# Optimization experiments

Measured on AMD Instinct MI355X. Metric: run time of the kernel, lower is better.

The kernel has to match this reference:

```python
import jax, jax.numpy as jnp
import numpy as np

EMBED = 256
PC_RANGE = np.array([-51.2, -51.2, -5.0, 51.2, 51.2, 3.0], np.float32)
INF_PC_RANGE = np.array([0.0, -51.2, -5.0, 102.4, 51.2, 3.0], np.float32)
EPS = 1e-5
NUM_THINGS = 3
THRESHOLD = 0.05


def _inverse_sigmoid(x):
    # mmdet inverse_sigmoid with eps=1e-5
    x = jnp.clip(x, 0.0, 1.0)
    x1 = jnp.clip(x, EPS, None)
    x2 = jnp.clip(1.0 - x, EPS, None)
    return jnp.log(x1 / x2)


def _norm2lidar(locs, pc_range):
    lo = jnp.asarray(pc_range[:3])
    hi = jnp.asarray(pc_range[3:])
    return locs * (hi - lo) + lo


def _lidar2norm(locs, pc_range):
    lo = jnp.asarray(pc_range[:3])
    hi = jnp.asarray(pc_range[3:])
    return (locs - lo) / (hi - lo)


def _transform(pts, calib):
    # pts [..., 3]; homogeneous transform with calib [4,4]
    h = jnp.concatenate([pts, jnp.ones_like(pts[..., :1])], -1)
    return jnp.einsum('ij,...j->...i', calib, h)[..., :3]


def setup_inputs() -> dict:
    key = jax.random.key(0)
    ks = jax.random.split(key, 16)
    L, BS, NI, NV, C = 6, 1, 8192, 16384, 3
    # logits shifted positive so sigmoid > 0.05 for every (query, class):
    # matching torch's duplicate-index gather semantics).
    inf_cls = jnp.abs(jax.random.normal(ks[0], (L, BS, NI, C), jnp.float32)) + 0.2
    inp = {
        'inf_outputs_classes': inf_cls,
        'inf_outputs_coords': jax.random.uniform(ks[1], (L, BS, NI, 4), jnp.float32),
        'inf_query': jax.random.normal(ks[2], (BS, NI, EMBED), jnp.float32),
        'inf_query_pos': jax.random.normal(ks[3], (BS, NI, EMBED), jnp.float32),
        'inf_reference': jax.random.normal(ks[4], (BS, NI, 4), jnp.float32),
        'veh_outputs_classes': jax.random.normal(ks[5], (L, BS, NV, C), jnp.float32),
        'veh_outputs_coords': jax.random.uniform(ks[6], (L, BS, NV, 4), jnp.float32),
        'veh_query': jax.random.normal(ks[7], (BS, NV, EMBED), jnp.float32),
        'veh_query_pos': jax.random.normal(ks[8], (BS, NV, EMBED), jnp.float32),
        'veh_reference': jax.random.normal(ks[9], (BS, NV, 4), jnp.float32),
    }
    # valid rigid inf->veh calibration T; module computes calib = inv(veh2inf_rt[0].T)
    th = 0.3
    T = np.eye(4, dtype=np.float64)
    T[:3, :3] = [[np.cos(th), -np.sin(th), 0.0], [np.sin(th), np.cos(th), 0.0], [0.0, 0.0, 1.0]]
    T[:3, 3] = [10.0, 2.0, 0.5]
    inp['veh2inf_rt'] = jnp.asarray(np.linalg.inv(T).T, jnp.float32)[None]
    s = 0.05
    inp['W_align'] = jax.random.normal(ks[10], (EMBED + 9, EMBED), jnp.float32) * s
    inp['b_align'] = jax.random.normal(ks[11], (EMBED,), jnp.float32) * s
    inp['W_align_pos'] = jax.random.normal(ks[12], (EMBED + 9, EMBED), jnp.float32) * s
    inp['b_align_pos'] = jax.random.normal(ks[13], (EMBED,), jnp.float32) * s
    return inp


def reference(inf_outputs_classes, inf_outputs_coords, inf_query, inf_query_pos,
              inf_reference, veh_outputs_classes, veh_outputs_coords, veh_query,
              veh_query_pos, veh_reference, veh2inf_rt, W_align, b_align,
              W_align_pos, b_align_pos):
    # calibration goes through numpy in the original -> constant, non-differentiable
    calib = jnp.asarray(np.linalg.inv(np.asarray(veh2inf_rt[0], np.float64).T), jnp.float32)

    # ---- filter_inf_lanes: threshold on last-layer sigmoid scores ----
    cls_score = jax.nn.sigmoid(inf_outputs_classes[-1])            # [bs, N, C]
    indexes = jnp.nonzero(cls_score.reshape(-1) > THRESHOLD)[0]
    bbox_index = indexes // NUM_THINGS                              # duplicates kept

    inf_outputs_classes = inf_outputs_classes[:, :, bbox_index, :]
    inf_outputs_coords = inf_outputs_coords[:, :, bbox_index, :]
    inf_query = inf_query[:, bbox_index, :]
    inf_query_pos = inf_query_pos[:, bbox_index, :]
    inf_reference = inf_reference[:, bbox_index, :]

    # ---- reference points: inf norm -> inf lidar -> veh lidar -> veh norm ----
    ref3 = jnp.concatenate([inf_reference[..., :2],
                            jnp.zeros_like(inf_reference[..., :1])], -1)  # [bs,N,3]
    locs = jax.nn.sigmoid(ref3)                    # _norm2lidar inverse_sigmoid mode
    locs = _norm2lidar(locs, INF_PC_RANGE)
    locs = _transform(locs, calib)
    locs = _inverse_sigmoid(_lidar2norm(locs, PC_RANGE))
    inf_reference = inf_reference.at[..., :2].set(locs[..., :2])

    # ---- per-layer bbox centers: same transform in sigmoid space ----
    bb3 = jnp.concatenate([inf_outputs_coords[..., :2],
                           jnp.zeros_like(inf_outputs_coords[..., :1])], -1)  # [L,bs,N,3]
    bb3 = _norm2lidar(bb3, INF_PC_RANGE)
    bb3 = _transform(bb3, calib)
    bb3 = _lidar2norm(bb3, PC_RANGE)
    inf_outputs_coords = inf_outputs_coords.at[..., :2].set(bb3[..., :2])

    # ---- cross-agent query alignment with rotation conditioning ----
    r = calib[:3, :3].reshape(9)
    r_b = jnp.broadcast_to(r, inf_query.shape[:-1] + (9,))
    inf_query = jnp.concatenate([inf_query, r_b], -1) @ W_align + b_align
    inf_query_pos = jnp.concatenate([inf_query_pos, r_b], -1) @ W_align_pos + b_align_pos

    # ---- complement vehicle-side sets with aligned inf lanes ----
    outputs_classes = jnp.concatenate([veh_outputs_classes, inf_outputs_classes], axis=2)
    outputs_coords = jnp.concatenate([veh_outputs_coords, inf_outputs_coords], axis=2)
    query = jnp.concatenate([veh_query, inf_query], axis=1)
    query_pos = jnp.concatenate([veh_query_pos, inf_query_pos], axis=1)
    reference = jnp.concatenate([veh_reference, inf_reference], axis=1)
    return (outputs_classes, outputs_coords, query, query_pos, reference)
```

## Files before the change

### kernel.cpp

```cpp
#include <hip/hip_runtime.h>
#include <hip/hip_bf16.h>

#define EMBED 256
#define LL 6

typedef __attribute__((ext_vector_type(8))) __bf16 bf16x8;
typedef __attribute__((ext_vector_type(4))) float f32x4;

#define SEL_THR (-2.9444389791664403f)

__global__ __launch_bounds__(1024) void k12(
        const float* __restrict__ cls, int n,
        const float* __restrict__ rt,
        const float* __restrict__ W0, const float* __restrict__ W1,
        const float* __restrict__ b0, const float* __restrict__ b1,
        float* __restrict__ calib,
        int* __restrict__ bbox, int* __restrict__ cnt,
        __bf16* __restrict__ Wt0, __bf16* __restrict__ Wt1,
        float* __restrict__ bvec0, float* __restrict__ bvec1) {
    int tid = threadIdx.x;

    if (blockIdx.x != 0) {
        int idx0 = blockIdx.x - 1;
        int which = idx0 >> 4;
        int t = idx0 & 15;
        int k0 = (t >> 2) * 64, c0 = (t & 3) * 64;
        const float* W = which ? W1 : W0;
        __bf16* Wt     = which ? Wt1 : Wt0;
        __shared__ float T[64][65];
#pragma unroll
        for (int i = 0; i < 4; ++i) {
            int idx = i * 1024 + tid;
            int kk = idx >> 6, cc = idx & 63;
            T[kk][cc] = W[(size_t)(k0 + kk) * EMBED + c0 + cc];
        }
        __syncthreads();
#pragma unroll
        for (int i = 0; i < 4; ++i) {
            int idx = i * 1024 + tid;
            int cc = idx >> 6, kk = idx & 63;
            Wt[(size_t)(c0 + cc) * EMBED + k0 + kk] = (__bf16)T[kk][cc];
        }
        return;
    }

    __shared__ int warpCnt[16];
    __shared__ float s_calib[16];
    int wid = tid >> 6, lane = tid & 63;

    if (tid == 0) {
        double a[4][8];
        for (int i = 0; i < 4; ++i)
            for (int j = 0; j < 4; ++j) {
                a[i][j]     = (double)rt[j * 4 + i];
                a[i][4 + j] = (i == j) ? 1.0 : 0.0;
            }
        for (int c = 0; c < 4; ++c) {
            int p = c; double best = fabs(a[c][c]);
            for (int r = c + 1; r < 4; ++r) { double v = fabs(a[r][c]); if (v > best) { best = v; p = r; } }
            if (p != c) for (int j = 0; j < 8; ++j) { double t2 = a[c][j]; a[c][j] = a[p][j]; a[p][j] = t2; }
            double inv = 1.0 / a[c][c];
            for (int j = 0; j < 8; ++j) a[c][j] *= inv;
            for (int r = 0; r < 4; ++r) if (r != c) {
                double f = a[r][c];
                for (int j = 0; j < 8; ++j) a[r][j] -= f * a[c][j];
            }
        }
        for (int i = 0; i < 4; ++i)
            for (int j = 0; j < 4; ++j) {
                float v = (float)a[i][4 + j];
                calib[i * 4 + j] = v;
                s_calib[i * 4 + j] = v;
            }
    }

    int PT = ((n + 1023) / 1024 + 3) & ~3;
    int PT4 = PT >> 2;
    int start = tid * PT;

    float4 v[16];
#pragma unroll
    for (int j4 = 0; j4 < 16; ++j4) {
        if (j4 < PT4) {
            int s = start + j4 * 4;
            if (s + 4 <= n) {
                v[j4] = *(const float4*)&cls[s];
            } else {
                float4 t2; t2.x = t2.y = t2.z = t2.w = -1e30f;
                if (s + 0 < n) t2.x = cls[s + 0];
                if (s + 1 < n) t2.y = cls[s + 1];
                if (s + 2 < n) t2.z = cls[s + 2];
                if (s + 3 < n) t2.w = cls[s + 3];
                v[j4] = t2;
            }
        }
    }
    int c = 0;
#pragma unroll
    for (int j4 = 0; j4 < 16; ++j4) {
        if (j4 < PT4) {
            c += (v[j4].x > SEL_THR) + (v[j4].y > SEL_THR) +
                 (v[j4].z > SEL_THR) + (v[j4].w > SEL_THR);
        }
    }
    int incl = c;
#pragma unroll
    for (int off = 1; off < 64; off <<= 1) {
        int u = __shfl_up(incl, off, 64);
        if (lane >= off) incl += u;
    }
    if (lane == 63) warpCnt[wid] = incl;
    __syncthreads();

    int base = 0;
    for (int w2 = 0; w2 < wid; ++w2) base += warpCnt[w2];
    int pos = base + incl - c;
#pragma unroll
    for (int j4 = 0; j4 < 16; ++j4) {
        if (j4 < PT4) {
            int s = start + j4 * 4;
            if (s + 0 < n && v[j4].x > SEL_THR) bbox[pos++] = (s + 0) / 3;
            if (s + 1 < n && v[j4].y > SEL_THR) bbox[pos++] = (s + 1) / 3;
            if (s + 2 < n && v[j4].z > SEL_THR) bbox[pos++] = (s + 2) / 3;
            if (s + 3 < n && v[j4].w > SEL_THR) bbox[pos++] = (s + 3) / 3;
        }
    }
    if (tid == 0) {
        int tot = 0;
        for (int w2 = 0; w2 < 16; ++w2) tot += warpCnt[w2];
        *cnt = tot;
    }

    if (tid < 512) {
        int which = tid >> 8;
        int j = tid & 255;
        const float* W = which ? W1 : W0;
        const float* b = which ? b1 : b0;
        float* o       = which ? bvec1 : bvec0;
        float s = b[j];
#pragma unroll
        for (int u = 0; u < 9; ++u) {
            float r = s_calib[(u / 3) * 4 + (u % 3)];
            s += r * W[(EMBED + u) * EMBED + j];
        }
        o[j] = s;
    }
}

__device__ __forceinline__ bf16x8 cvt8(float4 f0, float4 f1) {
    bf16x8 r;
    r[0] = (__bf16)f0.x; r[1] = (__bf16)f0.y; r[2] = (__bf16)f0.z; r[3] = (__bf16)f0.w;
    r[4] = (__bf16)f1.x; r[5] = (__bf16)f1.y; r[6] = (__bf16)f1.z; r[7] = (__bf16)f1.w;
    return r;
}

__global__ __launch_bounds__(256, 4) void k_gemm(
        const float* __restrict__ q0, const float* __restrict__ q1,
        const int* __restrict__ bbox,
        const __bf16* __restrict__ Wt0, const __bf16* __restrict__ Wt1,
        const float* __restrict__ bvec0, const float* __restrict__ bvec1,
        float* __restrict__ out, int NI, int K, int off0, int off1) {
    int g = blockIdx.y;
    const float* q    = g ? q1 : q0;
    const __bf16* Wt  = g ? Wt1 : Wt0;
    const float* bvec = g ? bvec1 : bvec0;
    int out_off       = g ? off1 : off0;

    int tid  = threadIdx.x;
    int w    = tid >> 6;
    int lane = tid & 63;
    int lo16 = lane & 15;
    int kg   = lane >> 4;
    int r0 = blockIdx.x * 64;

    const float* aptr[4];
#pragma unroll
    for (int t = 0; t < 4; ++t) {
        int row = r0 + 16 * t + lo16;
        int rc = min(row, K - 1);
        int box = bbox[rc]; box = max(0, min(box, NI - 1));
        aptr[t] = q + (size_t)box * EMBED + kg * 8;
    }
    const __bf16* bptr[4];
#pragma unroll
    for (int t = 0; t < 4; ++t) {
        int col = w * 64 + 16 * t + lo16;
        bptr[t] = Wt + (size_t)col * EMBED + kg * 8;
    }

    f32x4 acc[4][4];
#pragma unroll
    for (int ct = 0; ct < 4; ++ct) {
        float bv = bvec[w * 64 + 16 * ct + lo16];
#pragma unroll
        for (int rt = 0; rt < 4; ++rt) {
            acc[rt][ct][0] = bv; acc[rt][ct][1] = bv; acc[rt][ct][2] = bv; acc[rt][ct][3] = bv;
        }
    }
    for (int s = 0; s < 8; ++s) {
        bf16x8 a[4], b[4];
#pragma unroll
        for (int t = 0; t < 4; ++t) {
            float4 f0 = *(const float4*)(aptr[t] + s * 32);
            float4 f1 = *(const float4*)(aptr[t] + s * 32 + 4);
            a[t] = cvt8(f0, f1);
            b[t] = *(const bf16x8*)(bptr[t] + s * 32);
        }
#pragma unroll
        for (int rt = 0; rt < 4; ++rt)
#pragma unroll
            for (int ct = 0; ct < 4; ++ct)
                acc[rt][ct] = __builtin_amdgcn_mfma_f32_16x16x32_bf16(a[rt], b[ct], acc[rt][ct], 0, 0, 0);
    }
#pragma unroll
    for (int rt = 0; rt < 4; ++rt) {
#pragma unroll
        for (int reg = 0; reg < 4; ++reg) {
            int row = r0 + 16 * rt + kg * 4 + reg;
            if (row < K) {
#pragma unroll
                for (int ct = 0; ct < 4; ++ct) {
                    int col = w * 64 + 16 * ct + lo16;
                    out[out_off + (size_t)row * EMBED + col] = acc[rt][ct][reg];
                }
            }
        }
    }
}

struct Plan3 {
    const float* vsrc[5];
    const float* isrc[3];
    int start[9];
    int n4[5];
    int vdst[5];
    int idst[3];
    int perLay4[2];
    int layStride[2];
    int K, NI, NV, N;
};

__device__ __forceinline__ float inv_sig(float v) {
    v = fminf(fmaxf(v, 0.0f), 1.0f);
    float x1 = fmaxf(v, 1e-5f);
    float x2 = fmaxf(1.0f - v, 1e-5f);
    return logf(x1 / x2);
}

__global__ __launch_bounds__(256) void k3(Plan3 P, const int* __restrict__ bbox,
                                          const float* __restrict__ calib,
                                          float* __restrict__ out) {
    int bx = blockIdx.x;
    int j = 0;
    while (bx >= P.start[j + 1]) ++j;
    int lb  = bx - P.start[j];
    int tid = threadIdx.x;

    if (j < 5) {
        const int cmap[5] = {2, 3, 0, 1, 4};
        int cj = cmap[j];
#pragma unroll
        for (int it = 0; it < 4; ++it) {
            int i4 = lb * 1024 + it * 256 + tid;
            if (i4 < P.n4[cj]) {
                float4 v = *(const float4*)&P.vsrc[cj][(size_t)i4 * 4];
                size_t d;
                if (cj < 2) {
                    int l = i4 / P.perLay4[cj];
                    int r = i4 - l * P.perLay4[cj];
                    d = (size_t)P.vdst[cj] + (size_t)l * P.layStride[cj] + (size_t)r * 4;
                } else {
                    d = (size_t)P.vdst[cj] + (size_t)i4 * 4;
                }
                *(float4*)&out[d] = v;
            }
        }
        return;
    }

    int k = lb * 256 + tid;
    if (k >= P.K) return;
    int box = bbox[k]; box = max(0, min(box, P.NI - 1));

    if (j == 5) {
        const float* s0 = P.isrc[0];
#pragma unroll
        for (int l = 0; l < LL; ++l) {
            const float* s = s0 + ((size_t)l * P.NI + box) * 3;
            size_t d = (size_t)P.idst[0] + ((size_t)l * P.N + P.NV) * 3 + (size_t)k * 3;
            out[d + 0] = s[0]; out[d + 1] = s[1]; out[d + 2] = s[2];
        }
    } else if (j == 6) {
        float c00 = calib[0], c01 = calib[1], c03 = calib[3];
        float c10 = calib[4], c11 = calib[5], c13 = calib[7];
        float zx = calib[2] * -5.0f, zy = calib[6] * -5.0f;
#pragma unroll
        for (int l = 0; l < LL; ++l) {
            float4 s = *(const float4*)&P.isrc[1][((size_t)l * P.NI + box) * 4];
            float X = s.x * 102.4f;
            float Y = s.y * 102.4f - 51.2f;
            float tx = c00 * X + c01 * Y + zx + c03;
            float ty = c10 * X + c11 * Y + zy + c13;
            float4 v = make_float4((tx + 51.2f) * (1.0f / 102.4f),
                                   (ty + 51.2f) * (1.0f / 102.4f), s.z, s.w);
            *(float4*)&out[(size_t)P.idst[1] + ((size_t)l * P.N + P.NV + k) * 4] = v;
        }
    } else {
        float4 s = *(const float4*)&P.isrc[2][(size_t)box * 4];
        float sx = 1.0f / (1.0f + expf(-s.x));
        float sy = 1.0f / (1.0f + expf(-s.y));
        float X = sx * 102.4f;
        float Y = sy * 102.4f - 51.2f;
        float tx = calib[0] * X + calib[1] * Y + calib[2] * -1.0f + calib[3];
        float ty = calib[4] * X + calib[5] * Y + calib[6] * -1.0f + calib[7];
        float4 v = make_float4(inv_sig((tx + 51.2f) * (1.0f / 102.4f)),
                               inv_sig((ty + 51.2f) * (1.0f / 102.4f)), s.z, s.w);
        *(float4*)&out[(size_t)P.idst[2] + ((size_t)P.NV + k) * 4] = v;
    }
}

extern "C" void kernel_launch(void* const* d_in, const int* in_sizes, int n_in,
                              void* d_out, int out_size, void* d_ws, size_t ws_size,
                              hipStream_t stream) {
    const float* inf_cls   = (const float*)d_in[0];
    const float* inf_coord = (const float*)d_in[1];
    const float* inf_q     = (const float*)d_in[2];
    const float* inf_qp    = (const float*)d_in[3];
    const float* inf_ref   = (const float*)d_in[4];
    const float* veh_cls   = (const float*)d_in[5];
    const float* veh_coord = (const float*)d_in[6];
    const float* veh_q     = (const float*)d_in[7];
    const float* veh_qp    = (const float*)d_in[8];
    const float* veh_ref   = (const float*)d_in[9];
    const float* rt        = (const float*)d_in[10];
    const float* W0        = (const float*)d_in[11];
    const float* b0        = (const float*)d_in[12];
    const float* W1        = (const float*)d_in[13];
    const float* b1        = (const float*)d_in[14];
    float* out = (float*)d_out;

    int NI = in_sizes[0] / (LL * 3);
    int NV = in_sizes[5] / (LL * 3);
    int N  = out_size / 558;
    int K  = N - NV;

    int off_cls   = 0;
    int off_coord = LL * N * 3;
    int off_q     = off_coord + LL * N * 4;
    int off_qp    = off_q + N * EMBED;
    int off_ref   = off_qp + N * EMBED;

    char* ws = (char*)d_ws;
    float* calib = (float*)(ws);
    float* bvec0 = (float*)(ws + 128);
    float* bvec1 = (float*)(ws + 1152);
    int*   cnt   = (int*)(ws + 2176);
    int*   bbox  = (int*)(ws + 2304);
    __bf16* Wt0  = (__bf16*)(ws + 131072);
    __bf16* Wt1  = (__bf16*)(ws + 262144);

    hipLaunchKernelGGL(k12, dim3(33), dim3(1024), 0, stream,
                       inf_cls + (size_t)(LL - 1) * NI * 3, NI * 3, rt,
                       W0, W1, b0, b1, calib, bbox, cnt, Wt0, Wt1, bvec0, bvec1);

    if (K > 0) {
        hipLaunchKernelGGL(k_gemm, dim3((K + 63) / 64, 2), dim3(256), 0, stream,
                           inf_q, inf_qp, bbox, Wt0, Wt1, bvec0, bvec1,
                           out, NI, K, off_q + NV * EMBED, off_qp + NV * EMBED);
    }

    {
        Plan3 P;
        P.vsrc[0] = veh_cls; P.vsrc[1] = veh_coord; P.vsrc[2] = veh_q;
        P.vsrc[3] = veh_qp;  P.vsrc[4] = veh_ref;
        P.isrc[0] = inf_cls; P.isrc[1] = inf_coord; P.isrc[2] = inf_ref;
        P.n4[0] = LL * NV * 3 / 4;  P.n4[1] = LL * NV * 4 / 4;
        P.n4[2] = NV * EMBED / 4;   P.n4[3] = NV * EMBED / 4;  P.n4[4] = NV * 4 / 4;
        P.vdst[0] = off_cls; P.vdst[1] = off_coord; P.vdst[2] = off_q;
        P.vdst[3] = off_qp;  P.vdst[4] = off_ref;
        P.idst[0] = off_cls; P.idst[1] = off_coord; P.idst[2] = off_ref;
        P.perLay4[0] = NV * 3 / 4;  P.perLay4[1] = NV * 4 / 4;
        P.layStride[0] = N * 3;     P.layStride[1] = N * 4;
        P.K = K; P.NI = NI; P.NV = NV; P.N = N;

        int gblk = (K > 0) ? (K + 255) / 256 : 0;
        int nb[8];
        nb[0] = (P.n4[2] + 1023) / 1024;
        nb[1] = (P.n4[3] + 1023) / 1024;
        nb[2] = (P.n4[0] + 1023) / 1024;
        nb[3] = (P.n4[1] + 1023) / 1024;
        nb[4] = (P.n4[4] + 1023) / 1024;
        nb[5] = gblk; nb[6] = gblk; nb[7] = gblk;
        P.start[0] = 0;
        for (int j = 0; j < 8; ++j) P.start[j + 1] = P.start[j] + nb[j];
        if (P.start[8] > 0) {
            hipLaunchKernelGGL(k3, dim3(P.start[8]), dim3(256), 0, stream,
                               P, bbox, calib, out);
        }
    }
}
```

Measured before the change: 66.10 us.

## Shrink prep kernel to 256 threads and use grid-stride 2D copy kernel

```diff
diff --git a/kernel.cpp b/kernel.cpp
--- a/kernel.cpp
+++ b/kernel.cpp
@@ -8,8 +8,9 @@
 typedef __attribute__((ext_vector_type(4))) float f32x4;
 
 #define SEL_THR (-2.9444389791664403f)
-
-__global__ __launch_bounds__(1024) void k12(
+#define MAXPT4 32
+
+__global__ __launch_bounds__(256, 1) void k_prep(
         const float* __restrict__ cls, int n,
         const float* __restrict__ rt,
         const float* __restrict__ W0, const float* __restrict__ W1,
@@ -29,22 +30,22 @@
         __bf16* Wt     = which ? Wt1 : Wt0;
         __shared__ float T[64][65];
 #pragma unroll
-        for (int i = 0; i < 4; ++i) {
-            int idx = i * 1024 + tid;
+        for (int i = 0; i < 16; ++i) {
+            int idx = i * 256 + tid;
             int kk = idx >> 6, cc = idx & 63;
             T[kk][cc] = W[(size_t)(k0 + kk) * EMBED + c0 + cc];
         }
         __syncthreads();
 #pragma unroll
-        for (int i = 0; i < 4; ++i) {
-            int idx = i * 1024 + tid;
+        for (int i = 0; i < 16; ++i) {
+            int idx = i * 256 + tid;
             int cc = idx >> 6, kk = idx & 63;
             Wt[(size_t)(c0 + cc) * EMBED + k0 + kk] = (__bf16)T[kk][cc];
         }
         return;
     }
 
-    __shared__ int warpCnt[16];
+    __shared__ int warpCnt[4];
     __shared__ float s_calib[16];
     int wid = tid >> 6, lane = tid & 63;
 
@@ -74,13 +75,13 @@
             }
     }
 
-    int PT = ((n + 1023) / 1024 + 3) & ~3;
+    int PT = ((n + 255) / 256 + 3) & ~3;
     int PT4 = PT >> 2;
     int start = tid * PT;
 
-    float4 v[16];
-#pragma unroll
-    for (int j4 = 0; j4 < 16; ++j4) {
+    float4 v[MAXPT4];
+#pragma unroll
+    for (int j4 = 0; j4 < MAXPT4; ++j4) {
         if (j4 < PT4) {
             int s = start + j4 * 4;
             if (s + 4 <= n) {
@@ -97,7 +98,7 @@
     }
     int c = 0;
 #pragma unroll
-    for (int j4 = 0; j4 < 16; ++j4) {
+    for (int j4 = 0; j4 < MAXPT4; ++j4) {
         if (j4 < PT4) {
             c += (v[j4].x > SEL_THR) + (v[j4].y > SEL_THR) +
                  (v[j4].z > SEL_THR) + (v[j4].w > SEL_THR);
@@ -116,7 +117,7 @@
     for (int w2 = 0; w2 < wid; ++w2) base += warpCnt[w2];
     int pos = base + incl - c;
 #pragma unroll
-    for (int j4 = 0; j4 < 16; ++j4) {
+    for (int j4 = 0; j4 < MAXPT4; ++j4) {
         if (j4 < PT4) {
             int s = start + j4 * 4;
             if (s + 0 < n && v[j4].x > SEL_THR) bbox[pos++] = (s + 0) / 3;
@@ -127,23 +128,22 @@
     }
     if (tid == 0) {
         int tot = 0;
-        for (int w2 = 0; w2 < 16; ++w2) tot += warpCnt[w2];
+        for (int w2 = 0; w2 < 4; ++w2) tot += warpCnt[w2];
         *cnt = tot;
     }
 
-    if (tid < 512) {
-        int which = tid >> 8;
-        int j = tid & 255;
+#pragma unroll
+    for (int which = 0; which < 2; ++which) {
         const float* W = which ? W1 : W0;
         const float* b = which ? b1 : b0;
         float* o       = which ? bvec1 : bvec0;
-        float s = b[j];
+        float s = b[tid];
 #pragma unroll
         for (int u = 0; u < 9; ++u) {
             float r = s_calib[(u / 3) * 4 + (u % 3)];
-            s += r * W[(EMBED + u) * EMBED + j];
-        }
-        o[j] = s;
+            s += r * W[(EMBED + u) * EMBED + tid];
+        }
+        o[tid] = s;
     }
 }
 
@@ -228,15 +228,11 @@
     }
 }
 
-struct Plan3 {
-    const float* vsrc[5];
-    const float* isrc[3];
-    int start[9];
-    int n4[5];
-    int vdst[5];
-    int idst[3];
-    int perLay4[2];
-    int layStride[2];
+struct SJob { const float* src; int n4; int dstOff; int perLay4; int layStride; };
+struct PlanS {
+    SJob cj[5];
+    const float* icls; const float* icoord; const float* iref;
+    int dcls, dcoord, dref;
     int K, NI, NV, N;
 };
 
@@ -247,75 +243,68 @@
     return logf(x1 / x2);
 }
 
-__global__ __launch_bounds__(256) void k3(Plan3 P, const int* __restrict__ bbox,
-                                          const float* __restrict__ calib,
-                                          float* __restrict__ out) {
-    int bx = blockIdx.x;
-    int j = 0;
-    while (bx >= P.start[j + 1]) ++j;
-    int lb  = bx - P.start[j];
+__global__ __launch_bounds__(256) void k_stream(PlanS P, const int* __restrict__ bbox,
+                                                const float* __restrict__ calib,
+                                                float* __restrict__ out) {
+    int y = blockIdx.y;
     int tid = threadIdx.x;
 
-    if (j < 5) {
-        const int cmap[5] = {2, 3, 0, 1, 4};
-        int cj = cmap[j];
-#pragma unroll
-        for (int it = 0; it < 4; ++it) {
-            int i4 = lb * 1024 + it * 256 + tid;
-            if (i4 < P.n4[cj]) {
-                float4 v = *(const float4*)&P.vsrc[cj][(size_t)i4 * 4];
-                size_t d;
-                if (cj < 2) {
-                    int l = i4 / P.perLay4[cj];
-                    int r = i4 - l * P.perLay4[cj];
-                    d = (size_t)P.vdst[cj] + (size_t)l * P.layStride[cj] + (size_t)r * 4;
-                } else {
-                    d = (size_t)P.vdst[cj] + (size_t)i4 * 4;
-                }
-                *(float4*)&out[d] = v;
+    if (y < 5) {
+        SJob J = P.cj[y];
+        int stride = gridDim.x * 256;
+        if (J.layStride == 0) {
+            for (int i4 = blockIdx.x * 256 + tid; i4 < J.n4; i4 += stride) {
+                float4 v = *(const float4*)&J.src[(size_t)i4 * 4];
+                *(float4*)&out[(size_t)J.dstOff + (size_t)i4 * 4] = v;
+            }
+        } else {
+            for (int i4 = blockIdx.x * 256 + tid; i4 < J.n4; i4 += stride) {
+                int l = i4 / J.perLay4;
+                int r = i4 - l * J.perLay4;
+                float4 v = *(const float4*)&J.src[(size_t)i4 * 4];
+                *(float4*)&out[(size_t)J.dstOff + (size_t)l * J.layStride + (size_t)r * 4] = v;
             }
         }
         return;
     }
 
-    int k = lb * 256 + tid;
-    if (k >= P.K) return;
-    int box = bbox[k]; box = max(0, min(box, P.NI - 1));
-
-    if (j == 5) {
-        const float* s0 = P.isrc[0];
-#pragma unroll
-        for (int l = 0; l < LL; ++l) {
-            const float* s = s0 + ((size_t)l * P.NI + box) * 3;
-            size_t d = (size_t)P.idst[0] + ((size_t)l * P.N + P.NV) * 3 + (size_t)k * 3;
-            out[d + 0] = s[0]; out[d + 1] = s[1]; out[d + 2] = s[2];
-        }
-    } else if (j == 6) {
-        float c00 = calib[0], c01 = calib[1], c03 = calib[3];
-        float c10 = calib[4], c11 = calib[5], c13 = calib[7];
-        float zx = calib[2] * -5.0f, zy = calib[6] * -5.0f;
-#pragma unroll
-        for (int l = 0; l < LL; ++l) {
-            float4 s = *(const float4*)&P.isrc[1][((size_t)l * P.NI + box) * 4];
-            float X = s.x * 102.4f;
-            float Y = s.y * 102.4f - 51.2f;
-            float tx = c00 * X + c01 * Y + zx + c03;
-            float ty = c10 * X + c11 * Y + zy + c13;
-            float4 v = make_float4((tx + 51.2f) * (1.0f / 102.4f),
-                                   (ty + 51.2f) * (1.0f / 102.4f), s.z, s.w);
-            *(float4*)&out[(size_t)P.idst[1] + ((size_t)l * P.N + P.NV + k) * 4] = v;
-        }
-    } else {
-        float4 s = *(const float4*)&P.isrc[2][(size_t)box * 4];
-        float sx = 1.0f / (1.0f + expf(-s.x));
-        float sy = 1.0f / (1.0f + expf(-s.y));
-        float X = sx * 102.4f;
-        float Y = sy * 102.4f - 51.2f;
-        float tx = calib[0] * X + calib[1] * Y + calib[2] * -1.0f + calib[3];
-        float ty = calib[4] * X + calib[5] * Y + calib[6] * -1.0f + calib[7];
-        float4 v = make_float4(inv_sig((tx + 51.2f) * (1.0f / 102.4f)),
-                               inv_sig((ty + 51.2f) * (1.0f / 102.4f)), s.z, s.w);
-        *(float4*)&out[(size_t)P.idst[2] + ((size_t)P.NV + k) * 4] = v;
+    int stride = gridDim.x * 256;
+    for (int k = blockIdx.x * 256 + tid; k < P.K; k += stride) {
+        int box = bbox[k]; box = max(0, min(box, P.NI - 1));
+        if (y == 5) {
+#pragma unroll
+            for (int l = 0; l < LL; ++l) {
+                const float* s = P.icls + ((size_t)l * P.NI + box) * 3;
+                size_t d = (size_t)P.dcls + ((size_t)l * P.N + P.NV) * 3 + (size_t)k * 3;
+                out[d + 0] = s[0]; out[d + 1] = s[1]; out[d + 2] = s[2];
+            }
+        } else if (y == 6) {
+            float c00 = calib[0], c01 = calib[1], c03 = calib[3];
+            float c10 = calib[4], c11 = calib[5], c13 = calib[7];
+            float zx = calib[2] * -5.0f, zy = calib[6] * -5.0f;
+#pragma unroll
+            for (int l = 0; l < LL; ++l) {
+                float4 s = *(const float4*)&P.icoord[((size_t)l * P.NI + box) * 4];
+                float X = s.x * 102.4f;
+                float Y = s.y * 102.4f - 51.2f;
+                float tx = c00 * X + c01 * Y + zx + c03;
+                float ty = c10 * X + c11 * Y + zy + c13;
+                float4 v = make_float4((tx + 51.2f) * (1.0f / 102.4f),
+                                       (ty + 51.2f) * (1.0f / 102.4f), s.z, s.w);
+                *(float4*)&out[(size_t)P.dcoord + ((size_t)l * P.N + P.NV + k) * 4] = v;
+            }
+        } else {
+            float4 s = *(const float4*)&P.iref[(size_t)box * 4];
+            float sx = 1.0f / (1.0f + expf(-s.x));
+            float sy = 1.0f / (1.0f + expf(-s.y));
+            float X = sx * 102.4f;
+            float Y = sy * 102.4f - 51.2f;
+            float tx = calib[0] * X + calib[1] * Y + calib[2] * -1.0f + calib[3];
+            float ty = calib[4] * X + calib[5] * Y + calib[6] * -1.0f + calib[7];
+            float4 v = make_float4(inv_sig((tx + 51.2f) * (1.0f / 102.4f)),
+                                   inv_sig((ty + 51.2f) * (1.0f / 102.4f)), s.z, s.w);
+            *(float4*)&out[(size_t)P.dref + ((size_t)P.NV + k) * 4] = v;
+        }
     }
 }
 
@@ -359,7 +348,7 @@
     __bf16* Wt0  = (__bf16*)(ws + 131072);
     __bf16* Wt1  = (__bf16*)(ws + 262144);
 
-    hipLaunchKernelGGL(k12, dim3(33), dim3(1024), 0, stream,
+    hipLaunchKernelGGL(k_prep, dim3(33), dim3(256), 0, stream,
                        inf_cls + (size_t)(LL - 1) * NI * 3, NI * 3, rt,
                        W0, W1, b0, b1, calib, bbox, cnt, Wt0, Wt1, bvec0, bvec1);
 
@@ -370,32 +359,16 @@
     }
 
     {
-        Plan3 P;
-        P.vsrc[0] = veh_cls; P.vsrc[1] = veh_coord; P.vsrc[2] = veh_q;
-        P.vsrc[3] = veh_qp;  P.vsrc[4] = veh_ref;
-        P.isrc[0] = inf_cls; P.isrc[1] = inf_coord; P.isrc[2] = inf_ref;
-        P.n4[0] = LL * NV * 3 / 4;  P.n4[1] = LL * NV * 4 / 4;
-        P.n4[2] = NV * EMBED / 4;   P.n4[3] = NV * EMBED / 4;  P.n4[4] = NV * 4 / 4;
-        P.vdst[0] = off_cls; P.vdst[1] = off_coord; P.vdst[2] = off_q;
-        P.vdst[3] = off_qp;  P.vdst[4] = off_ref;
-        P.idst[0] = off_cls; P.idst[1] = off_coord; P.idst[2] = off_ref;
-        P.perLay4[0] = NV * 3 / 4;  P.perLay4[1] = NV * 4 / 4;
-        P.layStride[0] = N * 3;     P.layStride[1] = N * 4;
+        PlanS P;
+        P.cj[0] = { veh_q,     NV * EMBED / 4,  off_q,     NV * EMBED / 4, 0 };
+        P.cj[1] = { veh_qp,    NV * EMBED / 4,  off_qp,    NV * EMBED / 4, 0 };
+        P.cj[2] = { veh_cls,   LL * NV * 3 / 4, off_cls,   NV * 3 / 4,     N * 3 };
+        P.cj[3] = { veh_coord, LL * NV * 4 / 4, off_coord, NV * 4 / 4,     N * 4 };
+        P.cj[4] = { veh_ref,   NV * 4 / 4,      off_ref,   NV * 4 / 4,     0 };
+        P.icls = inf_cls; P.icoord = inf_coord; P.iref = inf_ref;
+        P.dcls = off_cls; P.dcoord = off_coord; P.dref = off_ref;
         P.K = K; P.NI = NI; P.NV = NV; P.N = N;
-
-        int gblk = (K > 0) ? (K + 255) / 256 : 0;
-        int nb[8];
-        nb[0] = (P.n4[2] + 1023) / 1024;
-        nb[1] = (P.n4[3] + 1023) / 1024;
-        nb[2] = (P.n4[0] + 1023) / 1024;
-        nb[3] = (P.n4[1] + 1023) / 1024;
-        nb[4] = (P.n4[4] + 1023) / 1024;
-        nb[5] = gblk; nb[6] = gblk; nb[7] = gblk;
-        P.start[0] = 0;
-        for (int j = 0; j < 8; ++j) P.start[j + 1] = P.start[j] + nb[j];
-        if (P.start[8] > 0) {
-            hipLaunchKernelGGL(k3, dim3(P.start[8]), dim3(256), 0, stream,
-                               P, bbox, calib, out);
-        }
-    }
-}
+        hipLaunchKernelGGL(k_stream, dim3(1024, 8), dim3(256), 0, stream,
+                           P, bbox, calib, out);
+    }
+}
```

New measurement: 71.19 us. 7.7% more time.
